# Kernel tuning notes

Measured on AMD Instinct MI355X. Metric: run time of the kernel, lower is better.

## Reference

```python
import jax, jax.numpy as jnp
import numpy as np

NB_VEC = 4  # module init arg nbVec
TEMP = 20.0  # distance temperature in exp(-d/20)


def setup_inputs() -> dict:
    key = jax.random.key(0)
    k1, k2 = jax.random.split(key)
    B, C, H, W = 16, 64, 256, 256
    x = jax.random.normal(k1, (B, C, H, W), dtype=jnp.float32)
    # stands in for torch.rand score init used when prior is None
    score_init = jax.random.uniform(k2, (B, H * W), dtype=jnp.float32)
    return {"x": x, "score_init": score_init}


def reference(x, score_init):
    B, C, H, W = x.shape
    N = H * W
    # [B, N, C] flattened spatial features
    xf = jnp.transpose(x, (0, 2, 3, 1)).reshape(B, N, C)
    batch = jnp.arange(B)
    score = score_init
    vecs, sims = [], []
    for _ in range(NB_VEC):
        ind = jnp.argmax(score, axis=1)                      # [B] greedy pick
        raw = xf[batch, ind]                                 # [B, C]
        d2 = jnp.sum((xf - raw[:, None, :]) ** 2, axis=-1)   # [B, N]
        # safe sqrt (distance is exactly 0 at the selected pixel)
        sim = jnp.exp(-jnp.sqrt(jnp.maximum(d2, 1e-12)) / TEMP)
        simNorm = sim / jnp.sum(sim, axis=1, keepdims=True)
        reprVec = jnp.einsum('bnc,bn->bc', xf, simNorm)      # softmax-weighted agg
        vecs.append(reprVec)
        sims.append(sim.reshape(B, 1, H, W))
        score = (1.0 - sim) * score                          # suppress nearby pts
    vecList = jnp.stack(vecs, axis=1)                        # [B, nbVec, C]
    simList = jnp.concatenate(sims, axis=1)                  # [B, nbVec, H, W]
    # selectedPos is only incremented in the onlySimSample branch; zeros here
    selectedPos = jnp.zeros((B, 1, H, W), dtype=x.dtype)
    return vecList, simList, selectedPos
```

## Files before the change

kernel.cpp:

```cpp
#include <hip/hip_runtime.h>

#define BB 16
#define CC 64
#define NN 65536
#define NBV 4
#define NPART 512
#define BP (BB * NPART)


__global__ __launch_bounds__(256)
void k_argmax1(const float* __restrict__ sc_in,
               float* __restrict__ bval, int* __restrict__ bidx,
               float* __restrict__ sel_out) {
    int b = blockIdx.y, blk = blockIdx.x, tid = threadIdx.x;
    int lane = tid & 63, wv = tid >> 6;
    int n0 = blk * 512 + tid * 2;
    const float* s = sc_in + (size_t)b * NN;
    float v0 = s[n0], v1 = s[n0 + 1];
    float v = v0; int vi = n0;
    if (v1 > v) { v = v1; vi = n0 + 1; }
    sel_out[(size_t)b * NN + n0] = 0.f;
    sel_out[(size_t)b * NN + n0 + 1] = 0.f;
    #pragma unroll
    for (int off = 32; off >= 1; off >>= 1) {
        float ov = __shfl_down(v, off, 64); int oi = __shfl_down(vi, off, 64);
        if (ov > v || (ov == v && oi < vi)) { v = ov; vi = oi; }
    }
    if (lane == 0) { bval[b * NPART + blk * 4 + wv] = v; bidx[b * NPART + blk * 4 + wv] = vi; }
}

__global__ __launch_bounds__(256, 2)
void k_iter(const float* __restrict__ x, const float* __restrict__ score_in,
            float* __restrict__ score_out,
            float* __restrict__ bval, int* __restrict__ bidx,
            float* __restrict__ wpart, float* __restrict__ sspart,
            float* __restrict__ sim_out, int iter) {
    int b = blockIdx.y, blk = blockIdx.x, tid = threadIdx.x;
    int lane = tid & 63, wv = tid >> 6;
    __shared__ float sv[256]; __shared__ int si[256];
    __shared__ float raw_s[64];

    int rb = (iter & 1) * BP, wb = ((iter & 1) ^ 1) * BP;

    {
        const float* bv = bval + rb + b * NPART;
        const int*  bi = bidx + rb + b * NPART;
        float v = bv[tid]; int vi = bi[tid];
        float v2 = bv[tid + 256]; int vi2 = bi[tid + 256];
        if (v2 > v || (v2 == v && vi2 < vi)) { v = v2; vi = vi2; }
        sv[tid] = v; si[tid] = vi;
        __syncthreads();
        for (int st = 128; st > 0; st >>= 1) {
            if (tid < st) {
                float ov = sv[tid + st]; int oi = si[tid + st];
                if (ov > sv[tid] || (ov == sv[tid] && oi < si[tid])) { sv[tid] = ov; si[tid] = oi; }
            }
            __syncthreads();
        }
    }
    int ind = si[0];
    if (tid < 64) raw_s[tid] = x[((size_t)(b * 64 + tid)) * NN + ind];
    __syncthreads();

    int p = blk * 4 + wv;
    int n0 = blk * 512 + wv * 128 + lane * 2;
    const float* xb = x + (size_t)b * 64 * NN + n0;
    const size_t sb = (size_t)b * NN;
    const bool upd = (iter < 3);

    float2 sc = make_float2(0.f, 0.f);
    if (upd) sc = *(const float2*)(score_in + sb + n0);

    float2 xv[64];
    #pragma unroll
    for (int c = 0; c < 64; c++) xv[c] = *(const float2*)(xb + (size_t)c * NN);
    float d2x = 0.f, d2y = 0.f;
    #pragma unroll
    for (int c = 0; c < 64; c++) {
        float r = raw_s[c];
        float dx = xv[c].x - r, dy = xv[c].y - r;
        d2x = fmaf(dx, dx, d2x); d2y = fmaf(dy, dy, d2y);
    }

    float simx = expf(-sqrtf(fmaxf(d2x, 1e-12f)) * 0.05f);
    float simy = expf(-sqrtf(fmaxf(d2y, 1e-12f)) * 0.05f);
    *(float2*)(sim_out + ((size_t)(b * NBV + iter)) * NN + n0) = make_float2(simx, simy);

    float ss = simx + simy;
    float smax = -1e30f; int smaxi = 0x7fffffff;
    if (upd) {
        float ncx = sc.x * (1.f - simx), ncy = sc.y * (1.f - simy);
        *(float2*)(score_out + sb + n0) = make_float2(ncx, ncy);
        smax = ncx; smaxi = n0;
        if (ncy > smax) { smax = ncy; smaxi = n0 + 1; }
    }

    float accl[64];
    #pragma unroll
    for (int c = 0; c < 64; c++) accl[c] = fmaf(simx, xv[c].x, simy * xv[c].y);

    #pragma unroll
    for (int c = 0; c < 64; c++) {
        float v = accl[c];
        #pragma unroll
        for (int off = 32; off >= 1; off >>= 1) v += __shfl_down(v, off, 64);
        if (lane == 0) wpart[((size_t)b * NPART + p) * 64 + c] = v;
    }
    #pragma unroll
    for (int off = 32; off >= 1; off >>= 1) ss += __shfl_down(ss, off, 64);
    if (lane == 0) sspart[b * NPART + p] = ss;
    if (upd) {
        #pragma unroll
        for (int off = 32; off >= 1; off >>= 1) {
            float ov = __shfl_down(smax, off, 64); int oi = __shfl_down(smaxi, off, 64);
            if (ov > smax || (ov == smax && oi < smaxi)) { smax = ov; smaxi = oi; }
        }
        if (lane == 0) { bval[wb + b * NPART + p] = smax; bidx[wb + b * NPART + p] = smaxi; }
    }
}

__global__ __launch_bounds__(256)
void k_fin(const float* __restrict__ wpart, const float* __restrict__ sspart,
           float* __restrict__ vec_out, int iter) {
    int b = blockIdx.x, tid = threadIdx.x;
    int c = tid & 63, q = tid >> 6;
    __shared__ float lw[4][64];
    __shared__ float lss[256];
    lss[tid] = sspart[b * NPART + 2 * tid] + sspart[b * NPART + 2 * tid + 1];
    float w = 0.f;
    for (int i = 0; i < 128; i++) {
        int pp = q * 128 + i;
        w += wpart[((size_t)b * NPART + pp) * 64 + c];
    }
    lw[q][c] = w;
    __syncthreads();
    for (int st = 128; st > 0; st >>= 1) {
        if (tid < st) lss[tid] += lss[tid + st];
        __syncthreads();
    }
    if (tid < 64) {
        float tot = (lw[0][tid] + lw[1][tid]) + (lw[2][tid] + lw[3][tid]);
        vec_out[(b * NBV + iter) * 64 + tid] = tot / lss[0];
    }
}

extern "C" void kernel_launch(void* const* d_in, const int* in_sizes, int n_in,
                              void* d_out, int out_size, void* d_ws, size_t ws_size,
                              hipStream_t stream) {
    const float* x = (const float*)d_in[0];
    const float* sc_in = (const float*)d_in[1];
    float* out = (float*)d_out;
    float* vec_out = out;
    float* sim_out = vec_out + (size_t)BB * NBV * CC;
    float* sel_out = sim_out + (size_t)BB * NBV * NN;

    float* ws = (float*)d_ws;
    float* score = ws;
    float* bval = ws + (size_t)BB * NN;
    int* bidx = (int*)(bval + 2 * BP);
    float* wpart = bval + 4 * BP;
    float* sspart = wpart + (size_t)BP * 64;

    k_argmax1<<<dim3(128, BB), 256, 0, stream>>>(sc_in, bval, bidx, sel_out);
    for (int it = 0; it < NBV; it++) {
        const float* s_in = (it == 0) ? sc_in : score;
        k_iter<<<dim3(128, BB), 256, 0, stream>>>(x, s_in, score, bval, bidx,
                                                  wpart, sspart, sim_out, it);
        k_fin<<<dim3(BB), 256, 0, stream>>>(wpart, sspart, vec_out, it);
    }
}
```

Measured before the change: 624.2 us.

## Transpose input to pixel-major layout and reduce weighted sums through LDS

Adds a one-time transpose of x into a [B,N,C] workspace buffer. The per-iteration kernel then gives each thread one pixel's 64 contiguous channels. The sim-weighted channel sums are reduced through a shared-memory tile instead of 64 chains of wave shuffles, which removes most of the cross-lane reduction work. The cost is an extra full read and write of x for the transpose and a large workspace requirement. If the workspace is too small, the old kernels are kept as a fallback path.

```diff
diff --git a/kernel.cpp b/kernel.cpp
--- a/kernel.cpp
+++ b/kernel.cpp
@@ -4,14 +4,188 @@
 #define CC 64
 #define NN 65536
 #define NBV 4
-#define NPART 512
-#define BP (BB * NPART)
-
+#define PNP 1024
+#define PBP (BB * PNP)
+#define FNP 512
+#define FBP (BB * FNP)
+
+
+
+__global__ __launch_bounds__(256)
+void k_transpose(const float* __restrict__ x, float* __restrict__ xt) {
+    int tile = blockIdx.x, h = blockIdx.y, b = blockIdx.z;
+    int t = threadIdx.x;
+    int c = t & 31, oct = t >> 5;
+    __shared__ float lds[256][36];
+    const float* src = x + ((size_t)(b * 64 + h * 32 + c)) * NN + tile * 256 + oct * 32;
+    float4 v[8];
+    #pragma unroll
+    for (int j = 0; j < 8; j++) v[j] = ((const float4*)src)[j];
+    #pragma unroll
+    for (int j = 0; j < 8; j++) {
+        lds[oct * 32 + j * 4 + 0][c] = v[j].x;
+        lds[oct * 32 + j * 4 + 1][c] = v[j].y;
+        lds[oct * 32 + j * 4 + 2][c] = v[j].z;
+        lds[oct * 32 + j * 4 + 3][c] = v[j].w;
+    }
+    __syncthreads();
+    float* dst = xt + ((size_t)b * NN + tile * 256 + t) * 64 + h * 32;
+    #pragma unroll
+    for (int k = 0; k < 8; k++) ((float4*)dst)[k] = *(const float4*)&lds[t][k * 4];
+}
 
 __global__ __launch_bounds__(256)
 void k_argmax1(const float* __restrict__ sc_in,
                float* __restrict__ bval, int* __restrict__ bidx,
                float* __restrict__ sel_out) {
+    int b = blockIdx.y, blk = blockIdx.x, tid = threadIdx.x;
+    int lane = tid & 63, wv = tid >> 6;
+    int n0 = blk * 256 + tid;
+    float v = sc_in[(size_t)b * NN + n0]; int vi = n0;
+    sel_out[(size_t)b * NN + n0] = 0.f;
+    #pragma unroll
+    for (int off = 32; off >= 1; off >>= 1) {
+        float ov = __shfl_down(v, off, 64); int oi = __shfl_down(vi, off, 64);
+        if (ov > v || (ov == v && oi < vi)) { v = ov; vi = oi; }
+    }
+    if (lane == 0) { bval[b * PNP + blk * 4 + wv] = v; bidx[b * PNP + blk * 4 + wv] = vi; }
+}
+
+__global__ __launch_bounds__(256, 2)
+void k_iter_t(const float* __restrict__ xt, const float* __restrict__ score_in,
+              float* __restrict__ score_out,
+              float* __restrict__ bval, int* __restrict__ bidx,
+              float* __restrict__ wpart, float* __restrict__ sspart,
+              float* __restrict__ sim_out, int iter) {
+    int b = blockIdx.y, blk = blockIdx.x, tid = threadIdx.x;
+    int lane = tid & 63, wv = tid >> 6;
+    __shared__ float sv[256]; __shared__ int si[256];
+    __shared__ float raw_s[64];
+    __shared__ float lacc[256][33];
+    __shared__ float lq[8][32];
+
+    int rb = (iter & 1) * PBP, wb = ((iter & 1) ^ 1) * PBP;
+
+    {
+        const float* bv = bval + rb + b * PNP;
+        const int* bi = bidx + rb + b * PNP;
+        float v = bv[tid]; int vi = bi[tid];
+        #pragma unroll
+        for (int s = 1; s < 4; s++) {
+            float ov = bv[tid + 256 * s]; int oi = bi[tid + 256 * s];
+            if (ov > v || (ov == v && oi < vi)) { v = ov; vi = oi; }
+        }
+        sv[tid] = v; si[tid] = vi;
+        __syncthreads();
+        for (int st = 128; st > 0; st >>= 1) {
+            if (tid < st) {
+                float ov = sv[tid + st]; int oi = si[tid + st];
+                if (ov > sv[tid] || (ov == sv[tid] && oi < si[tid])) { sv[tid] = ov; si[tid] = oi; }
+            }
+            __syncthreads();
+        }
+    }
+    int ind = si[0];
+    if (tid < 64) raw_s[tid] = xt[((size_t)b * NN + ind) * 64 + tid];
+    __syncthreads();
+
+    int n0 = blk * 256 + tid;
+    const float4* xp = (const float4*)(xt + ((size_t)b * NN + n0) * 64);
+    float4 xa[16];
+    #pragma unroll
+    for (int j = 0; j < 16; j++) xa[j] = xp[j];
+
+    float d2 = 0.f;
+    #pragma unroll
+    for (int j = 0; j < 16; j++) {
+        float4 r4 = *(const float4*)&raw_s[j * 4];
+        float dx = xa[j].x - r4.x, dy = xa[j].y - r4.y;
+        float dz = xa[j].z - r4.z, dw = xa[j].w - r4.w;
+        d2 = fmaf(dx, dx, d2); d2 = fmaf(dy, dy, d2);
+        d2 = fmaf(dz, dz, d2); d2 = fmaf(dw, dw, d2);
+    }
+    float sim = expf(-sqrtf(fmaxf(d2, 1e-12f)) * 0.05f);
+
+    const size_t sb = (size_t)b * NN;
+    sim_out[((size_t)(b * NBV + iter)) * NN + n0] = sim;
+    const bool upd = (iter < 3);
+    float ss = sim, smax = -1e30f; int smaxi = n0;
+    if (upd) {
+        float nc = score_in[sb + n0] * (1.f - sim);
+        score_out[sb + n0] = nc;
+        smax = nc;
+    }
+
+    #pragma unroll
+    for (int h = 0; h < 2; h++) {
+        #pragma unroll
+        for (int j = 0; j < 8; j++) {
+            float4 xv4 = xa[h * 8 + j];
+            lacc[tid][j * 4 + 0] = sim * xv4.x;
+            lacc[tid][j * 4 + 1] = sim * xv4.y;
+            lacc[tid][j * 4 + 2] = sim * xv4.z;
+            lacc[tid][j * 4 + 3] = sim * xv4.w;
+        }
+        __syncthreads();
+        int c = tid & 31, oct = tid >> 5;
+        float s = 0.f;
+        #pragma unroll
+        for (int r = 0; r < 32; r++) s += lacc[oct * 32 + r][c];
+        lq[oct][c] = s;
+        __syncthreads();
+        if (tid < 32) {
+            float t4 = 0.f;
+            #pragma unroll
+            for (int o = 0; o < 8; o++) t4 += lq[o][tid];
+            wpart[((size_t)b * 256 + blk) * 64 + h * 32 + tid] = t4;
+        }
+        __syncthreads();
+    }
+
+    #pragma unroll
+    for (int off = 32; off >= 1; off >>= 1) ss += __shfl_down(ss, off, 64);
+    if (lane == 0) sspart[b * PNP + blk * 4 + wv] = ss;
+    if (upd) {
+        float v = smax; int idx = smaxi;
+        #pragma unroll
+        for (int off = 32; off >= 1; off >>= 1) {
+            float ov = __shfl_down(v, off, 64); int oi = __shfl_down(idx, off, 64);
+            if (ov > v || (ov == v && oi < idx)) { v = ov; idx = oi; }
+        }
+        if (lane == 0) { bval[wb + b * PNP + blk * 4 + wv] = v; bidx[wb + b * PNP + blk * 4 + wv] = idx; }
+    }
+}
+
+__global__ __launch_bounds__(256)
+void k_fin(const float* __restrict__ wpart, const float* __restrict__ sspart,
+           float* __restrict__ vec_out, int iter) {
+    int b = blockIdx.x, tid = threadIdx.x;
+    int c = tid & 63, q = tid >> 6;
+    __shared__ float lw[4][64];
+    __shared__ float lss[256];
+    float s4 = 0.f;
+    #pragma unroll
+    for (int i = 0; i < 4; i++) s4 += sspart[b * PNP + i * 256 + tid];
+    lss[tid] = s4;
+    float w = 0.f;
+    for (int i = 0; i < 64; i++) w += wpart[((size_t)b * 256 + q * 64 + i) * 64 + c];
+    lw[q][c] = w;
+    __syncthreads();
+    for (int st = 128; st > 0; st >>= 1) {
+        if (tid < st) lss[tid] += lss[tid + st];
+        __syncthreads();
+    }
+    if (tid < 64) {
+        float tot = (lw[0][tid] + lw[1][tid]) + (lw[2][tid] + lw[3][tid]);
+        vec_out[(b * NBV + iter) * 64 + tid] = tot / lss[0];
+    }
+}
+
+
+__global__ __launch_bounds__(256)
+void k_argmax1_fb(const float* __restrict__ sc_in,
+                  float* __restrict__ bval, int* __restrict__ bidx,
+                  float* __restrict__ sel_out) {
     int b = blockIdx.y, blk = blockIdx.x, tid = threadIdx.x;
     int lane = tid & 63, wv = tid >> 6;
     int n0 = blk * 512 + tid * 2;
@@ -26,25 +200,23 @@
         float ov = __shfl_down(v, off, 64); int oi = __shfl_down(vi, off, 64);
         if (ov > v || (ov == v && oi < vi)) { v = ov; vi = oi; }
     }
-    if (lane == 0) { bval[b * NPART + blk * 4 + wv] = v; bidx[b * NPART + blk * 4 + wv] = vi; }
+    if (lane == 0) { bval[b * FNP + blk * 4 + wv] = v; bidx[b * FNP + blk * 4 + wv] = vi; }
 }
 
 __global__ __launch_bounds__(256, 2)
-void k_iter(const float* __restrict__ x, const float* __restrict__ score_in,
-            float* __restrict__ score_out,
-            float* __restrict__ bval, int* __restrict__ bidx,
-            float* __restrict__ wpart, float* __restrict__ sspart,
-            float* __restrict__ sim_out, int iter) {
+void k_iter_fb(const float* __restrict__ x, const float* __restrict__ score_in,
+               float* __restrict__ score_out,
+               float* __restrict__ bval, int* __restrict__ bidx,
+               float* __restrict__ wpart, float* __restrict__ sspart,
+               float* __restrict__ sim_out, int iter) {
     int b = blockIdx.y, blk = blockIdx.x, tid = threadIdx.x;
     int lane = tid & 63, wv = tid >> 6;
     __shared__ float sv[256]; __shared__ int si[256];
     __shared__ float raw_s[64];
-
-    int rb = (iter & 1) * BP, wb = ((iter & 1) ^ 1) * BP;
-
+    int rb = (iter & 1) * FBP, wb = ((iter & 1) ^ 1) * FBP;
     {
-        const float* bv = bval + rb + b * NPART;
-        const int*  bi = bidx + rb + b * NPART;
+        const float* bv = bval + rb + b * FNP;
+        const int* bi = bidx + rb + b * FNP;
         float v = bv[tid]; int vi = bi[tid];
         float v2 = bv[tid + 256]; int vi2 = bi[tid + 256];
         if (v2 > v || (v2 == v && vi2 < vi)) { v = v2; vi = vi2; }
@@ -61,16 +233,13 @@
     int ind = si[0];
     if (tid < 64) raw_s[tid] = x[((size_t)(b * 64 + tid)) * NN + ind];
     __syncthreads();
-
     int p = blk * 4 + wv;
     int n0 = blk * 512 + wv * 128 + lane * 2;
     const float* xb = x + (size_t)b * 64 * NN + n0;
     const size_t sb = (size_t)b * NN;
     const bool upd = (iter < 3);
-
     float2 sc = make_float2(0.f, 0.f);
     if (upd) sc = *(const float2*)(score_in + sb + n0);
-
     float2 xv[64];
     #pragma unroll
     for (int c = 0; c < 64; c++) xv[c] = *(const float2*)(xb + (size_t)c * NN);
@@ -81,11 +250,9 @@
         float dx = xv[c].x - r, dy = xv[c].y - r;
         d2x = fmaf(dx, dx, d2x); d2y = fmaf(dy, dy, d2y);
     }
-
     float simx = expf(-sqrtf(fmaxf(d2x, 1e-12f)) * 0.05f);
     float simy = expf(-sqrtf(fmaxf(d2y, 1e-12f)) * 0.05f);
     *(float2*)(sim_out + ((size_t)(b * NBV + iter)) * NN + n0) = make_float2(simx, simy);
-
     float ss = simx + simy;
     float smax = -1e30f; int smaxi = 0x7fffffff;
     if (upd) {
@@ -94,44 +261,39 @@
         smax = ncx; smaxi = n0;
         if (ncy > smax) { smax = ncy; smaxi = n0 + 1; }
     }
-
     float accl[64];
     #pragma unroll
     for (int c = 0; c < 64; c++) accl[c] = fmaf(simx, xv[c].x, simy * xv[c].y);
-
     #pragma unroll
     for (int c = 0; c < 64; c++) {
         float v = accl[c];
         #pragma unroll
         for (int off = 32; off >= 1; off >>= 1) v += __shfl_down(v, off, 64);
-        if (lane == 0) wpart[((size_t)b * NPART + p) * 64 + c] = v;
+        if (lane == 0) wpart[((size_t)b * FNP + p) * 64 + c] = v;
     }
     #pragma unroll
     for (int off = 32; off >= 1; off >>= 1) ss += __shfl_down(ss, off, 64);
-    if (lane == 0) sspart[b * NPART + p] = ss;
+    if (lane == 0) sspart[b * FNP + p] = ss;
     if (upd) {
         #pragma unroll
         for (int off = 32; off >= 1; off >>= 1) {
             float ov = __shfl_down(smax, off, 64); int oi = __shfl_down(smaxi, off, 64);
             if (ov > smax || (ov == smax && oi < smaxi)) { smax = ov; smaxi = oi; }
         }
-        if (lane == 0) { bval[wb + b * NPART + p] = smax; bidx[wb + b * NPART + p] = smaxi; }
-    }
-}
-
-__global__ __launch_bounds__(256)
-void k_fin(const float* __restrict__ wpart, const float* __restrict__ sspart,
-           float* __restrict__ vec_out, int iter) {
+        if (lane == 0) { bval[wb + b * FNP + p] = smax; bidx[wb + b * FNP + p] = smaxi; }
+    }
+}
+
+__global__ __launch_bounds__(256)
+void k_fin_fb(const float* __restrict__ wpart, const float* __restrict__ sspart,
+              float* __restrict__ vec_out, int iter) {
     int b = blockIdx.x, tid = threadIdx.x;
     int c = tid & 63, q = tid >> 6;
     __shared__ float lw[4][64];
     __shared__ float lss[256];
-    lss[tid] = sspart[b * NPART + 2 * tid] + sspart[b * NPART + 2 * tid + 1];
+    lss[tid] = sspart[b * FNP + 2 * tid] + sspart[b * FNP + 2 * tid + 1];
     float w = 0.f;
-    for (int i = 0; i < 128; i++) {
-        int pp = q * 128 + i;
-        w += wpart[((size_t)b * NPART + pp) * 64 + c];
-    }
+    for (int i = 0; i < 128; i++) w += wpart[((size_t)b * FNP + q * 128 + i) * 64 + c];
     lw[q][c] = w;
     __syncthreads();
     for (int st = 128; st > 0; st >>= 1) {
@@ -156,16 +318,35 @@
 
     float* ws = (float*)d_ws;
     float* score = ws;
+
     float* bval = ws + (size_t)BB * NN;
-    int* bidx = (int*)(bval + 2 * BP);
-    float* wpart = bval + 4 * BP;
-    float* sspart = wpart + (size_t)BP * 64;
-
-    k_argmax1<<<dim3(128, BB), 256, 0, stream>>>(sc_in, bval, bidx, sel_out);
-    for (int it = 0; it < NBV; it++) {
-        const float* s_in = (it == 0) ? sc_in : score;
-        k_iter<<<dim3(128, BB), 256, 0, stream>>>(x, s_in, score, bval, bidx,
-                                                  wpart, sspart, sim_out, it);
-        k_fin<<<dim3(BB), 256, 0, stream>>>(wpart, sspart, vec_out, it);
-    }
-}
+    int* bidx = (int*)(bval + 2 * PBP);
+    float* wpart = bval + 4 * PBP;
+    float* sspart = wpart + (size_t)BB * 256 * 64;
+    float* xt = sspart + PBP;
+    size_t need = ((size_t)BB * NN + 4 * PBP + (size_t)BB * 256 * 64 + PBP
+                   + (size_t)BB * NN * 64) * sizeof(float);
+
+    if (ws_size >= need) {
+        k_transpose<<<dim3(256, 2, BB), 256, 0, stream>>>(x, xt);
+        k_argmax1<<<dim3(256, BB), 256, 0, stream>>>(sc_in, bval, bidx, sel_out);
+        for (int it = 0; it < NBV; it++) {
+            const float* s_in = (it == 0) ? sc_in : score;
+            k_iter_t<<<dim3(256, BB), 256, 0, stream>>>(xt, s_in, score, bval, bidx,
+                                                        wpart, sspart, sim_out, it);
+            k_fin<<<dim3(BB), 256, 0, stream>>>(wpart, sspart, vec_out, it);
+        }
+    } else {
+        float* fbval = ws + (size_t)BB * NN;
+        int* fbidx = (int*)(fbval + 2 * FBP);
+        float* fwpart = fbval + 4 * FBP;
+        float* fsspart = fwpart + (size_t)FBP * 64;
+        k_argmax1_fb<<<dim3(128, BB), 256, 0, stream>>>(sc_in, fbval, fbidx, sel_out);
+        for (int it = 0; it < NBV; it++) {
+            const float* s_in = (it == 0) ? sc_in : score;
+            k_iter_fb<<<dim3(128, BB), 256, 0, stream>>>(x, s_in, score, fbval, fbidx,
+                                                         fwpart, fsspart, sim_out, it);
+            k_fin_fb<<<dim3(BB), 256, 0, stream>>>(fwpart, fsspart, vec_out, it);
+        }
+    }
+}
```

After: 706.9 us. 1.13x slower.
